# Kernel optimization log

Hardware: AMD Instinct MI355X
Metric: run time of the kernel (lower is better)

The kernel has to match this reference:

```python
import math
import jax, jax.numpy as jnp
from jax import lax
import numpy as np

LN_EPS = 1e-5
K = 3          # deform-conv kernel size
PAD = 1        # 'same' padding so offset map matches output resolution


def setup_inputs() -> dict:
    key = jax.random.key(0)
    ks = jax.random.split(key, 6)
    B, C, H, W, Co = 4, 256, 64, 64, 256
    x = jax.random.normal(ks[0], (B, C, H, W), jnp.float32)
    dwc_w = jax.random.normal(ks[1], (C, 1, K, K), jnp.float32) * 0.02
    ln_w = jnp.ones((C,), jnp.float32)
    ln_b = jnp.zeros((C,), jnp.float32)
    fcd_w = jax.random.normal(ks[2], (1, C, 1, 1), jnp.float32) * 0.02
    fca_w = jax.random.normal(ks[3], (1, C, 1, 1), jnp.float32) * 0.02
    fan_in = C * K * K
    dconv_w = jax.random.normal(ks[4], (Co, C, K, K), jnp.float32) / math.sqrt(fan_in)
    dconv_b = jnp.zeros((Co,), jnp.float32)
    return dict(x=x, dwc_w=dwc_w, ln_w=ln_w, ln_b=ln_b,
                fcd_w=fcd_w, fca_w=fca_w, dconv_w=dconv_w, dconv_b=dconv_b)


def _bilinear_sample(x, py, px):
    # x: [B,C,H,W]; py/px: [B,KK,H,W] float sample positions (zero-padded border)
    B, C, H, W = x.shape
    y0 = jnp.floor(py); x0 = jnp.floor(px)
    y1 = y0 + 1.0;      x1 = x0 + 1.0
    wy1 = py - y0; wy0 = 1.0 - wy1
    wx1 = px - x0; wx0 = 1.0 - wx1

    def gather(yy, xx):
        valid = ((yy >= 0) & (yy < H) & (xx >= 0) & (xx < W)).astype(x.dtype)
        iy = jnp.clip(yy, 0, H - 1).astype(jnp.int32)
        ix = jnp.clip(xx, 0, W - 1).astype(jnp.int32)
        # per-batch fancy gather -> [B,C,KK,H,W]
        v = jax.vmap(lambda img, a, b: img[:, a, b])(x, iy, ix)
        return v * valid[:, None]

    return (gather(y0, x0) * (wy0 * wx0)[:, None]
          + gather(y0, x1) * (wy0 * wx1)[:, None]
          + gather(y1, x0) * (wy1 * wx0)[:, None]
          + gather(y1, x1) * (wy1 * wx1)[:, None])


def reference(x, dwc_w, ln_w, ln_b, fcd_w, fca_w, dconv_w, dconv_b):
    B, C, H, W = x.shape
    KK = K * K
    # --- offset branch ---
    h = lax.conv_general_dilated(x, dwc_w, (1, 1), ((1, 1), (1, 1)),
                                 dimension_numbers=('NCHW', 'OIHW', 'NCHW'),
                                 feature_group_count=C)
    mu = h.mean(axis=1, keepdims=True)
    var = h.var(axis=1, keepdims=True)
    h = (h - mu) * lax.rsqrt(var + LN_EPS)
    h = h * ln_w[None, :, None, None] + ln_b[None, :, None, None]
    h = jax.nn.relu(h)
    r = jax.nn.relu(jnp.einsum('bchw,oc->bohw', h, fcd_w[:, :, 0, 0]))      # [B,1,H,W]
    t = jnp.einsum('bchw,oc->bohw', h, fca_w[:, :, 0, 0])
    theta = (t / (1.0 + jnp.abs(t))) * (math.pi / 180.0)                     # softsign * pi/180
    ox = r * jnp.cos(theta)
    oy = r * jnp.sin(theta)
    # torch code: offsets = cat([ox tiled KK, oy tiled KK], dim=1) -> [B,2KK,H,W]
    off = jnp.concatenate([jnp.tile(ox, (1, KK, 1, 1)), jnp.tile(oy, (1, KK, 1, 1))], axis=1)
    # torchvision DeformConv2d convention: channel 2k = dy, channel 2k+1 = dx
    dy = off[:, 0::2]   # [B,KK,H,W]
    dx = off[:, 1::2]
    # --- deformable sampling ---
    ky = jnp.repeat(jnp.arange(K), K).astype(x.dtype)   # kernel row per tap
    kx = jnp.tile(jnp.arange(K), K).astype(x.dtype)     # kernel col per tap
    py = (jnp.arange(H, dtype=x.dtype) - PAD)[None, None, :, None] + ky[None, :, None, None] + dy
    px = (jnp.arange(W, dtype=x.dtype) - PAD)[None, None, None, :] + kx[None, :, None, None] + dx
    sampled = _bilinear_sample(x, py, px)               # [B,C,KK,H,W]
    Co = dconv_w.shape[0]
    out = jnp.einsum('bckhw,ock->bohw', sampled, dconv_w.reshape(Co, C, KK))
    return out + dconv_b[None, :, None, None]
```

## Files before the change

kernel.cpp:

```cpp
#include <hip/hip_runtime.h>
#include <hip/hip_bf16.h>

#define B_   4
#define C_   256
#define CO_  256
#define H_   64
#define W_   64
#define HW_  4096

typedef __attribute__((ext_vector_type(8))) short short8;
typedef __attribute__((ext_vector_type(4))) float f32x4;
typedef __attribute__((ext_vector_type(2))) float f32x2;

static __device__ __forceinline__ unsigned short f2bf(float f) {
    unsigned u = __builtin_bit_cast(unsigned, f);
    unsigned r = (u + 0x7fffu + ((u >> 16) & 1u)) >> 16;
    return (unsigned short)r;
}
static __device__ __forceinline__ f32x2 pk_mul(f32x2 a, f32x2 b) {
    f32x2 d; asm("v_pk_mul_f32 %0, %1, %2" : "=v"(d) : "v"(a), "v"(b)); return d;
}
static __device__ __forceinline__ f32x2 pk_fma(f32x2 a, f32x2 b, f32x2 c) {
    f32x2 d; asm("v_pk_fma_f32 %0, %1, %2, %3" : "=v"(d) : "v"(a), "v"(b), "v"(c)); return d;
}
static __device__ __forceinline__ f32x2 pk_add(f32x2 a, f32x2 b) {
    f32x2 d; asm("v_pk_add_f32 %0, %1, %2" : "=v"(d) : "v"(a), "v"(b)); return d;
}
static __device__ __forceinline__ unsigned cvtpk(float a, float b) {
    unsigned r; asm("v_cvt_pk_bf16_f32 %0, %1, %2" : "=v"(r) : "v"(a), "v"(b)); return r;
}
static __device__ __forceinline__ f32x2 unpack_bf2(unsigned d) {
    f32x2 v;
    v.x = __builtin_bit_cast(float, d << 16);
    v.y = __builtin_bit_cast(float, d & 0xffff0000u);
    return v;
}

__global__ void k_pre(const float* __restrict__ x, unsigned short* __restrict__ xT,
                      const float* __restrict__ w, unsigned short* __restrict__ Bt,
                      const float* __restrict__ dwc_w, float* __restrict__ dwcT)
{
    int bid = blockIdx.x;
    int tid = threadIdx.x;
    if (bid < 1024) {
        __shared__ float t[32][132];
        int b   = bid >> 8;
        int rem = bid & 255;
        int hwT = rem >> 1, cT = rem & 1;
        int hw0 = hwT * 32, c0 = cT * 128;
        const float* src = x + (size_t)b * C_ * HW_;
        {
            int hw4 = (tid & 7) << 2;
            int cr  = tid >> 3;
#pragma unroll
            for (int it = 0; it < 4; ++it) {
                int c = cr + it * 32;
                f32x4 v = *(const f32x4*)(src + (size_t)(c0 + c) * HW_ + hw0 + hw4);
                t[hw4 + 0][c] = v.x;
                t[hw4 + 1][c] = v.y;
                t[hw4 + 2][c] = v.z;
                t[hw4 + 3][c] = v.w;
            }
        }
        __syncthreads();
        {
            int c8  = (tid & 15) << 3;
            int hwr = tid >> 4;
            unsigned short* dst = xT + (size_t)(((b << 12) + hw0) * 256) + c0 + c8;
#pragma unroll
            for (int it = 0; it < 2; ++it) {
                int hw = hwr + it * 16;
                f32x4 va = *(const f32x4*)&t[hw][c8];
                f32x4 vb = *(const f32x4*)&t[hw][c8 + 4];
                uint4 u;
                u.x = cvtpk(va.x, va.y);
                u.y = cvtpk(va.z, va.w);
                u.z = cvtpk(vb.x, vb.y);
                u.w = cvtpk(vb.z, vb.w);
                *(uint4*)(dst + (size_t)hw * 256) = u;
            }
        }
    } else {
        int pb = bid - 1024;
        if (pb < 9) dwcT[pb * 256 + tid] = dwc_w[tid * 9 + pb];
        int e = pb * 256 + tid;
        int j   = e & 7;
        int l4  = (e >> 3) & 3;
        int l15 = (e >> 5) & 15;
        int ks  = (e >> 9) & 7;
        int og  = (e >> 12) & 15;
        int k   = e >> 16;
        int o = og * 16 + l15;
        int c = ks * 32 + l4 * 8 + j;
        Bt[e] = f2bf(w[(o * C_ + c) * 9 + k]);
    }
}

__global__ void k_offsets(const unsigned short* __restrict__ xT,
                          const float* __restrict__ dwcT,
                          const float* __restrict__ ln_w,
                          const float* __restrict__ ln_b,
                          const float* __restrict__ fcd_w,
                          const float* __restrict__ fca_w,
                          float* __restrict__ OX, float* __restrict__ OY)
{
    int tid = threadIdx.x;
    int bi = blockIdx.x;
    int g = ((bi & 7) << 6) | (bi >> 3);
    int p0 = g << 5;
    int b = p0 >> 12;
    int y = (p0 >> 6) & 63;
    int xh = p0 & 63;
    int gpos = tid >> 4;
    int csub = tid & 15;
    int ch0 = csub << 4;
    const unsigned short* xb = xT + (size_t)b * HW_ * C_;

    f32x2 acc2[8];
#pragma unroll
    for (int i = 0; i < 8; ++i) { acc2[i].x = 0.f; acc2[i].y = 0.f; }
#pragma unroll
    for (int j = 0; j < 9; ++j) {
        int gy = y + j / 3 - 1, gx = xh + gpos + j % 3 - 1;
        if (gy >= 0 && gy < H_ && gx >= 0 && gx < W_) {
            const unsigned short* p = xb + (size_t)((gy << 6) + gx) * 256 + ch0;
            short8 rlo = *(const short8*)(p);
            short8 rhi = *(const short8*)(p + 8);
            const float* wrow = dwcT + j * 256 + ch0;
#pragma unroll
            for (int q = 0; q < 4; ++q) {
                f32x4 wv = *(const f32x4*)(wrow + q * 4);
                f32x2 w01v; w01v.x = wv.x; w01v.y = wv.y;
                f32x2 w23v; w23v.x = wv.z; w23v.y = wv.w;
                unsigned lo = (q < 2) ? ((unsigned*)&rlo)[q * 2] : ((unsigned*)&rhi)[(q - 2) * 2];
                unsigned hi = (q < 2) ? ((unsigned*)&rlo)[q * 2 + 1] : ((unsigned*)&rhi)[(q - 2) * 2 + 1];
                acc2[q * 2 + 0] = pk_fma(unpack_bf2(lo), w01v, acc2[q * 2 + 0]);
                acc2[q * 2 + 1] = pk_fma(unpack_bf2(hi), w23v, acc2[q * 2 + 1]);
            }
        }
    }
    f32x2 sum2, sq2;
    sum2.x = 0.f; sum2.y = 0.f; sq2.x = 0.f; sq2.y = 0.f;
#pragma unroll
    for (int i = 0; i < 8; ++i) {
        sum2 = pk_add(sum2, acc2[i]);
        sq2  = pk_fma(acc2[i], acc2[i], sq2);
    }
    float s1 = sum2.x + sum2.y, s2 = sq2.x + sq2.y;
#pragma unroll
    for (int m = 1; m <= 8; m <<= 1) {
        s1 += __shfl_xor(s1, m);
        s2 += __shfl_xor(s2, m);
    }
    float mu  = s1 * (1.f / 256.f);
    float var = s2 * (1.f / 256.f) - mu * mu;
    float rs  = rsqrtf(var + 1e-5f);
    float d1 = 0.f, d2 = 0.f;
#pragma unroll
    for (int q = 0; q < 4; ++q) {
        f32x4 lwv = *(const f32x4*)(ln_w  + ch0 + q * 4);
        f32x4 lbv = *(const f32x4*)(ln_b  + ch0 + q * 4);
        f32x4 fdv = *(const f32x4*)(fcd_w + ch0 + q * 4);
        f32x4 fav = *(const f32x4*)(fca_w + ch0 + q * 4);
#pragma unroll
        for (int i = 0; i < 4; ++i) {
            float av = (i & 1) ? acc2[q * 2 + (i >> 1)].y : acc2[q * 2 + (i >> 1)].x;
            float hn = (av - mu) * rs * lwv[i] + lbv[i];
            hn = fmaxf(hn, 0.f);
            d1 = fmaf(hn, fdv[i], d1);
            d2 = fmaf(hn, fav[i], d2);
        }
    }
#pragma unroll
    for (int m = 1; m <= 8; m <<= 1) {
        d1 += __shfl_xor(d1, m);
        d2 += __shfl_xor(d2, m);
    }
    if (csub == 0) {
        float r0 = fmaxf(d1, 0.f);
        float theta = d2 / (1.f + fabsf(d2)) * 0.017453292519943295f;
        int pos = p0 + gpos;
        OX[pos] = r0 * cosf(theta);
        OY[pos] = r0 * sinf(theta);
    }
}

__launch_bounds__(512, 4)
__global__ void k_main(const unsigned short* __restrict__ xT,
                       const float* __restrict__ OX, const float* __restrict__ OY,
                       const unsigned short* __restrict__ Bt,
                       const float* __restrict__ bias,
                       float* __restrict__ out)
{
    __shared__ __align__(16) unsigned char smem[32768];

    int tid = threadIdx.x;
    int bi = blockIdx.x;
    int g = ((bi & 7) << 6) | (bi >> 3);
    int tile = g >> 1;
    int n0g = g & 1;
    int b = tile >> 6;
    int y = tile & 63;

    int lane = tid & 63, wid = tid >> 6;
    int l15 = lane & 15, l4 = lane >> 4;

    f32x4 acc[4];
#pragma unroll
    for (int m = 0; m < 4; ++m) {
        acc[m].x = 0.f; acc[m].y = 0.f; acc[m].z = 0.f; acc[m].w = 0.f;
    }

    int gpos = tid >> 3;
    unsigned csub = (unsigned)tid & 7u;
    const char* xbB = (const char*)(xT + (size_t)b * HW_ * C_);
    const unsigned short* bwave = Bt + (unsigned)(n0g * 8 + wid) * 4096u
                                     + (unsigned)(l15 * 32 + l4 * 8);
    unsigned rowb = (unsigned)gpos * 256u;
    unsigned wsl0 = (csub ^ ((unsigned)gpos & 15u)) << 4;
    unsigned wsl1 = ((8u + csub) ^ ((unsigned)gpos & 15u)) << 4;
    float ox = OX[(tile << 6) + gpos], oy = OY[(tile << 6) + gpos];

    unsigned o00, o01, o10, o11;
    f32x2 W00, W01, W10, W11;

#define GADDR(k)                                                                  \
    {   int ky = (k) / 3, kx = (k) - ky * 3;                                      \
        float dyv = ((k) <= 4) ? ox : oy;                                         \
        float dxv = ((k) <= 3) ? ox : oy;                                         \
        float py = (float)(y - 1 + ky) + dyv;                                     \
        float px = (float)(gpos - 1 + kx) + dxv;                                  \
        float y0f = floorf(py), x0f = floorf(px);                                 \
        int y0 = (int)y0f, x0 = (int)x0f;                                         \
        int y1 = y0 + 1, x1 = x0 + 1;                                             \
        float wy1 = py - y0f, wy0 = 1.f - wy1;                                    \
        float wx1 = px - x0f, wx0 = 1.f - wx1;                                    \
        float vy0 = (y0 >= 0 && y0 < H_) ? 1.f : 0.f;                             \
        float vy1 = (y1 >= 0 && y1 < H_) ? 1.f : 0.f;                             \
        float vx0 = (x0 >= 0 && x0 < W_) ? 1.f : 0.f;                             \
        float vx1 = (x1 >= 0 && x1 < W_) ? 1.f : 0.f;                             \
        float w00 = wy0 * wx0 * vy0 * vx0, w01 = wy0 * wx1 * vy0 * vx1;           \
        float w10 = wy1 * wx0 * vy1 * vx0, w11 = wy1 * wx1 * vy1 * vx1;           \
        W00.x = w00; W00.y = w00; W01.x = w01; W01.y = w01;                       \
        W10.x = w10; W10.y = w10; W11.x = w11; W11.y = w11;                       \
        int y0c = min(max(y0, 0), H_ - 1), y1c = min(max(y1, 0), H_ - 1);         \
        int x0c = min(max(x0, 0), W_ - 1), x1c = min(max(x1, 0), W_ - 1);         \
        unsigned cb = csub << 4;                                                  \
        o00 = (unsigned)((y0c << 6) + x0c) * 512u + cb;                           \
        o01 = (unsigned)((y0c << 6) + x1c) * 512u + cb;                           \
        o10 = (unsigned)((y1c << 6) + x0c) * 512u + cb;                           \
        o11 = (unsigned)((y1c << 6) + x1c) * 512u + cb;                           \
    }

#define GATHER_HALF(h, hbase)                                                     \
    {   _Pragma("unroll")                                                         \
        for (int cq2 = 0; cq2 < 2; ++cq2) {                                       \
            unsigned gb = (unsigned)(h) * 256u + (unsigned)cq2 * 128u;            \
            short8 r00 = *(const short8*)(xbB + o00 + gb);                        \
            short8 r01 = *(const short8*)(xbB + o01 + gb);                        \
            short8 r10 = *(const short8*)(xbB + o10 + gb);                        \
            short8 r11 = *(const short8*)(xbB + o11 + gb);                        \
            uint4 pkv;                                                            \
            _Pragma("unroll")                                                     \
            for (int dw = 0; dw < 4; ++dw) {                                      \
                f32x2 a2 = pk_mul(unpack_bf2(((unsigned*)&r00)[dw]), W00);        \
                a2 = pk_fma(unpack_bf2(((unsigned*)&r01)[dw]), W01, a2);          \
                a2 = pk_fma(unpack_bf2(((unsigned*)&r10)[dw]), W10, a2);          \
                a2 = pk_fma(unpack_bf2(((unsigned*)&r11)[dw]), W11, a2);          \
                ((unsigned*)&pkv)[dw] = cvtpk(a2.x, a2.y);                        \
            }                                                                     \
            *(uint4*)(smem + (hbase) + rowb + (cq2 ? wsl1 : wsl0)) = pkv;         \
        }                                                                         \
    }

#define MFMA_HALF(k, h, hbase)                                                    \
    {   const unsigned short* bk = bwave + (unsigned)(k) * 65536u;                \
        _Pragma("unroll")                                                         \
        for (int ks2 = 0; ks2 < 4; ++ks2) {                                       \
            int ks = (h) * 4 + ks2;                                               \
            short8 bf = *(const short8*)(bk + ks * 512);                          \
            unsigned sl = ((unsigned)(ks2 * 4 + l4) ^ (unsigned)l15) << 4;        \
            _Pragma("unroll")                                                     \
            for (int mf = 0; mf < 4; ++mf) {                                      \
                unsigned row = (unsigned)(mf * 16 + l15);                         \
                short8 a = *(const short8*)(smem + (hbase) + row * 256u + sl);    \
                acc[mf] = __builtin_amdgcn_mfma_f32_16x16x32_bf16(a, bf, acc[mf], 0, 0, 0); \
            }                                                                     \
        }                                                                         \
    }

    GADDR(0);
    GATHER_HALF(0, 0u);
    __syncthreads();

#pragma unroll
    for (int k = 0; k < 9; ++k) {
        GATHER_HALF(1, 16384u);
        MFMA_HALF(k, 0, 0u);
        __syncthreads();
        if (k < 8) {
            GADDR(k + 1);
            GATHER_HALF(0, 0u);
        }
        MFMA_HALF(k, 1, 16384u);
        __syncthreads();
    }

    int col = n0g * 128 + wid * 16 + l15;
    float bv = bias[col];
    float* obase = out + ((size_t)(b * CO_ + col)) * HW_ + (y << 6);
#pragma unroll
    for (int mf = 0; mf < 4; ++mf) {
        f32x4 v;
        v.x = acc[mf].x + bv;
        v.y = acc[mf].y + bv;
        v.z = acc[mf].z + bv;
        v.w = acc[mf].w + bv;
        *(f32x4*)(obase + mf * 16 + l4 * 4) = v;
    }
}

extern "C" void kernel_launch(void* const* d_in, const int* in_sizes, int n_in,
                              void* d_out, int out_size, void* d_ws, size_t ws_size,
                              hipStream_t stream) {
    const float* x      = (const float*)d_in[0];
    const float* dwc_w  = (const float*)d_in[1];
    const float* ln_w   = (const float*)d_in[2];
    const float* ln_b   = (const float*)d_in[3];
    const float* fcd_w  = (const float*)d_in[4];
    const float* fca_w  = (const float*)d_in[5];
    const float* dconv_w= (const float*)d_in[6];
    const float* dconv_b= (const float*)d_in[7];
    float* out = (float*)d_out;

    unsigned char* ws = (unsigned char*)d_ws;
    unsigned short* xT = (unsigned short*)(ws);
    unsigned short* Bt = (unsigned short*)(ws + 8388608);
    float* dwcT        = (float*)(ws + 9568256);
    float* OX          = (float*)(ws + 9577472);
    float* OY          = (float*)(ws + 9643008);

    k_pre<<<3328, 256, 0, stream>>>(x, xT, dconv_w, Bt, dwc_w, dwcT);
    k_offsets<<<512, 512, 0, stream>>>(xT, dwcT, ln_w, ln_b, fcd_w, fca_w, OX, OY);
    k_main<<<512, 512, 0, stream>>>(xT, OX, OY, Bt, dconv_b, out);
}
```

Baseline: 73.49 us.

## Retile deform-conv main kernel to 32-pixel by 256-channel tiles with 1024 threads

```diff
diff --git a/kernel.cpp b/kernel.cpp
--- a/kernel.cpp
+++ b/kernel.cpp
@@ -185,7 +185,7 @@
     }
 }
 
-__launch_bounds__(512, 4)
+__launch_bounds__(1024, 8)
 __global__ void k_main(const unsigned short* __restrict__ xT,
                        const float* __restrict__ OX, const float* __restrict__ OY,
                        const unsigned short* __restrict__ Bt,
@@ -197,29 +197,28 @@
     int tid = threadIdx.x;
     int bi = blockIdx.x;
     int g = ((bi & 7) << 6) | (bi >> 3);
-    int tile = g >> 1;
-    int n0g = g & 1;
-    int b = tile >> 6;
-    int y = tile & 63;
+    int p0 = g << 5;
+    int b = p0 >> 12;
+    int y = (p0 >> 6) & 63;
+    int xh = p0 & 63;
 
     int lane = tid & 63, wid = tid >> 6;
     int l15 = lane & 15, l4 = lane >> 4;
 
-    f32x4 acc[4];
-#pragma unroll
-    for (int m = 0; m < 4; ++m) {
+    f32x4 acc[2];
+#pragma unroll
+    for (int m = 0; m < 2; ++m) {
         acc[m].x = 0.f; acc[m].y = 0.f; acc[m].z = 0.f; acc[m].w = 0.f;
     }
 
-    int gpos = tid >> 3;
-    unsigned csub = (unsigned)tid & 7u;
+    int gpos = tid >> 5;
+    unsigned csub = (unsigned)tid & 31u;
     const char* xbB = (const char*)(xT + (size_t)b * HW_ * C_);
-    const unsigned short* bwave = Bt + (unsigned)(n0g * 8 + wid) * 4096u
+    const unsigned short* bwave = Bt + (unsigned)wid * 4096u
                                      + (unsigned)(l15 * 32 + l4 * 8);
-    unsigned rowb = (unsigned)gpos * 256u;
-    unsigned wsl0 = (csub ^ ((unsigned)gpos & 15u)) << 4;
-    unsigned wsl1 = ((8u + csub) ^ ((unsigned)gpos & 15u)) << 4;
-    float ox = OX[(tile << 6) + gpos], oy = OY[(tile << 6) + gpos];
+    unsigned rowb = (unsigned)gpos * 512u;
+    unsigned wsl  = (csub ^ ((unsigned)gpos & 15u)) << 4;
+    float ox = OX[p0 + gpos], oy = OY[p0 + gpos];
 
     unsigned o00, o01, o10, o11;
     f32x2 W00, W01, W10, W11;
@@ -229,7 +228,7 @@
         float dyv = ((k) <= 4) ? ox : oy;                                         \
         float dxv = ((k) <= 3) ? ox : oy;                                         \
         float py = (float)(y - 1 + ky) + dyv;                                     \
-        float px = (float)(gpos - 1 + kx) + dxv;                                  \
+        float px = (float)(xh + gpos - 1 + kx) + dxv;                             \
         float y0f = floorf(py), x0f = floorf(px);                                 \
         int y0 = (int)y0f, x0 = (int)x0f;                                         \
         int y1 = y0 + 1, x1 = x0 + 1;                                             \
@@ -252,65 +251,59 @@
         o11 = (unsigned)((y1c << 6) + x1c) * 512u + cb;                           \
     }
 
-#define GATHER_HALF(h, hbase)                                                     \
-    {   _Pragma("unroll")                                                         \
-        for (int cq2 = 0; cq2 < 2; ++cq2) {                                       \
-            unsigned gb = (unsigned)(h) * 256u + (unsigned)cq2 * 128u;            \
-            short8 r00 = *(const short8*)(xbB + o00 + gb);                        \
-            short8 r01 = *(const short8*)(xbB + o01 + gb);                        \
-            short8 r10 = *(const short8*)(xbB + o10 + gb);                        \
-            short8 r11 = *(const short8*)(xbB + o11 + gb);                        \
-            uint4 pkv;                                                            \
-            _Pragma("unroll")                                                     \
-            for (int dw = 0; dw < 4; ++dw) {                                      \
-                f32x2 a2 = pk_mul(unpack_bf2(((unsigned*)&r00)[dw]), W00);        \
-                a2 = pk_fma(unpack_bf2(((unsigned*)&r01)[dw]), W01, a2);          \
-                a2 = pk_fma(unpack_bf2(((unsigned*)&r10)[dw]), W10, a2);          \
-                a2 = pk_fma(unpack_bf2(((unsigned*)&r11)[dw]), W11, a2);          \
-                ((unsigned*)&pkv)[dw] = cvtpk(a2.x, a2.y);                        \
-            }                                                                     \
-            *(uint4*)(smem + (hbase) + rowb + (cq2 ? wsl1 : wsl0)) = pkv;         \
+#define GATHER_TAP(hbase)                                                         \
+    {   short8 r00 = *(const short8*)(xbB + o00);                                 \
+        short8 r01 = *(const short8*)(xbB + o01);                                 \
+        short8 r10 = *(const short8*)(xbB + o10);                                 \
+        short8 r11 = *(const short8*)(xbB + o11);                                 \
+        uint4 pkv;                                                                \
+        _Pragma("unroll")                                                         \
+        for (int dw = 0; dw < 4; ++dw) {                                          \
+            f32x2 a2 = pk_mul(unpack_bf2(((unsigned*)&r00)[dw]), W00);            \
+            a2 = pk_fma(unpack_bf2(((unsigned*)&r01)[dw]), W01, a2);              \
+            a2 = pk_fma(unpack_bf2(((unsigned*)&r10)[dw]), W10, a2);              \
+            a2 = pk_fma(unpack_bf2(((unsigned*)&r11)[dw]), W11, a2);              \
+            ((unsigned*)&pkv)[dw] = cvtpk(a2.x, a2.y);                            \
         }                                                                         \
-    }
-
-#define MFMA_HALF(k, h, hbase)                                                    \
+        *(uint4*)(smem + (hbase) + rowb + wsl) = pkv;                             \
+    }
+
+#define MFMA_TAP(k, hbase)                                                        \
     {   const unsigned short* bk = bwave + (unsigned)(k) * 65536u;                \
         _Pragma("unroll")                                                         \
-        for (int ks2 = 0; ks2 < 4; ++ks2) {                                       \
-            int ks = (h) * 4 + ks2;                                               \
+        for (int ks = 0; ks < 8; ++ks) {                                          \
             short8 bf = *(const short8*)(bk + ks * 512);                          \
-            unsigned sl = ((unsigned)(ks2 * 4 + l4) ^ (unsigned)l15) << 4;        \
+            unsigned sl = ((unsigned)(ks * 4 + l4) ^ (unsigned)l15) << 4;         \
             _Pragma("unroll")                                                     \
-            for (int mf = 0; mf < 4; ++mf) {                                      \
+            for (int mf = 0; mf < 2; ++mf) {                                      \
                 unsigned row = (unsigned)(mf * 16 + l15);                         \
-                short8 a = *(const short8*)(smem + (hbase) + row * 256u + sl);    \
+                short8 a = *(const short8*)(smem + (hbase) + row * 512u + sl);    \
                 acc[mf] = __builtin_amdgcn_mfma_f32_16x16x32_bf16(a, bf, acc[mf], 0, 0, 0); \
             }                                                                     \
         }                                                                         \
     }
 
     GADDR(0);
-    GATHER_HALF(0, 0u);
+    GATHER_TAP(0u);
     __syncthreads();
 
 #pragma unroll
     for (int k = 0; k < 9; ++k) {
-        GATHER_HALF(1, 16384u);
-        MFMA_HALF(k, 0, 0u);
-        __syncthreads();
+        unsigned cur = (k & 1) ? 16384u : 0u;
+        unsigned nxt = (k & 1) ? 0u : 16384u;
         if (k < 8) {
             GADDR(k + 1);
-            GATHER_HALF(0, 0u);
-        }
-        MFMA_HALF(k, 1, 16384u);
+            GATHER_TAP(nxt);
+        }
+        MFMA_TAP(k, cur);
         __syncthreads();
     }
 
-    int col = n0g * 128 + wid * 16 + l15;
+    int col = wid * 16 + l15;
     float bv = bias[col];
-    float* obase = out + ((size_t)(b * CO_ + col)) * HW_ + (y << 6);
-#pragma unroll
-    for (int mf = 0; mf < 4; ++mf) {
+    float* obase = out + ((size_t)(b * CO_ + col)) * HW_ + (y << 6) + xh;
+#pragma unroll
+    for (int mf = 0; mf < 2; ++mf) {
         f32x4 v;
         v.x = acc[mf].x + bv;
         v.y = acc[mf].y + bv;
@@ -342,5 +335,5 @@
 
     k_pre<<<3328, 256, 0, stream>>>(x, xT, dconv_w, Bt, dwc_w, dwcT);
     k_offsets<<<512, 512, 0, stream>>>(xT, dwcT, ln_w, ln_b, fcd_w, fca_w, OX, OY);
-    k_main<<<512, 512, 0, stream>>>(xT, OX, OY, Bt, dconv_b, out);
-}
+    k_main<<<512, 1024, 0, stream>>>(xT, OX, OY, Bt, dconv_b, out);
+}
```

After: 80.25 us. +9.2%, slower.

## Compute all output channels per block and double-buffer full-tap gathers

Applied to the files above, without the earlier changes.

```diff
diff --git a/kernel.cpp b/kernel.cpp
--- a/kernel.cpp
+++ b/kernel.cpp
@@ -185,36 +185,36 @@
     }
 }
 
-__launch_bounds__(512, 4)
+__launch_bounds__(512, 2)
 __global__ void k_main(const unsigned short* __restrict__ xT,
                        const float* __restrict__ OX, const float* __restrict__ OY,
                        const unsigned short* __restrict__ Bt,
                        const float* __restrict__ bias,
                        float* __restrict__ out)
 {
-    __shared__ __align__(16) unsigned char smem[32768];
+    __shared__ __align__(16) unsigned char smem[65536];
 
     int tid = threadIdx.x;
     int bi = blockIdx.x;
-    int g = ((bi & 7) << 6) | (bi >> 3);
-    int tile = g >> 1;
-    int n0g = g & 1;
+    int tile = ((bi & 7) << 5) | (bi >> 3);
     int b = tile >> 6;
     int y = tile & 63;
 
     int lane = tid & 63, wid = tid >> 6;
     int l15 = lane & 15, l4 = lane >> 4;
 
-    f32x4 acc[4];
-#pragma unroll
-    for (int m = 0; m < 4; ++m) {
-        acc[m].x = 0.f; acc[m].y = 0.f; acc[m].z = 0.f; acc[m].w = 0.f;
-    }
+    f32x4 acc[4][2];
+#pragma unroll
+    for (int m = 0; m < 4; ++m)
+#pragma unroll
+        for (int n = 0; n < 2; ++n) {
+            acc[m][n].x = 0.f; acc[m][n].y = 0.f; acc[m][n].z = 0.f; acc[m][n].w = 0.f;
+        }
 
     int gpos = tid >> 3;
     unsigned csub = (unsigned)tid & 7u;
     const char* xbB = (const char*)(xT + (size_t)b * HW_ * C_);
-    const unsigned short* bwave = Bt + (unsigned)(n0g * 8 + wid) * 4096u
+    const unsigned short* bwave = Bt + (unsigned)(wid * 2) * 4096u
                                      + (unsigned)(l15 * 32 + l4 * 8);
     unsigned rowb = (unsigned)gpos * 256u;
     unsigned wsl0 = (csub ^ ((unsigned)gpos & 15u)) << 4;
@@ -278,45 +278,52 @@
         _Pragma("unroll")                                                         \
         for (int ks2 = 0; ks2 < 4; ++ks2) {                                       \
             int ks = (h) * 4 + ks2;                                               \
-            short8 bf = *(const short8*)(bk + ks * 512);                          \
+            short8 bf0 = *(const short8*)(bk + ks * 512);                         \
+            short8 bf1 = *(const short8*)(bk + 4096 + ks * 512);                  \
             unsigned sl = ((unsigned)(ks2 * 4 + l4) ^ (unsigned)l15) << 4;        \
             _Pragma("unroll")                                                     \
             for (int mf = 0; mf < 4; ++mf) {                                      \
                 unsigned row = (unsigned)(mf * 16 + l15);                         \
                 short8 a = *(const short8*)(smem + (hbase) + row * 256u + sl);    \
-                acc[mf] = __builtin_amdgcn_mfma_f32_16x16x32_bf16(a, bf, acc[mf], 0, 0, 0); \
+                acc[mf][0] = __builtin_amdgcn_mfma_f32_16x16x32_bf16(a, bf0, acc[mf][0], 0, 0, 0); \
+                acc[mf][1] = __builtin_amdgcn_mfma_f32_16x16x32_bf16(a, bf1, acc[mf][1], 0, 0, 0); \
             }                                                                     \
         }                                                                         \
     }
 
     GADDR(0);
     GATHER_HALF(0, 0u);
+    GATHER_HALF(1, 16384u);
     __syncthreads();
 
 #pragma unroll
     for (int k = 0; k < 9; ++k) {
-        GATHER_HALF(1, 16384u);
-        MFMA_HALF(k, 0, 0u);
-        __syncthreads();
+        unsigned cur = (k & 1) ? 32768u : 0u;
+        unsigned nxt = (k & 1) ? 0u : 32768u;
         if (k < 8) {
             GADDR(k + 1);
-            GATHER_HALF(0, 0u);
-        }
-        MFMA_HALF(k, 1, 16384u);
+            GATHER_HALF(0, nxt);
+            GATHER_HALF(1, nxt + 16384u);
+        }
+        MFMA_HALF(k, 0, cur);
+        MFMA_HALF(k, 1, cur + 16384u);
         __syncthreads();
     }
 
-    int col = n0g * 128 + wid * 16 + l15;
-    float bv = bias[col];
-    float* obase = out + ((size_t)(b * CO_ + col)) * HW_ + (y << 6);
-#pragma unroll
-    for (int mf = 0; mf < 4; ++mf) {
-        f32x4 v;
-        v.x = acc[mf].x + bv;
-        v.y = acc[mf].y + bv;
-        v.z = acc[mf].z + bv;
-        v.w = acc[mf].w + bv;
-        *(f32x4*)(obase + mf * 16 + l4 * 4) = v;
+#pragma unroll
+    for (int nf = 0; nf < 2; ++nf) {
+        int col = wid * 32 + nf * 16 + l15;
+        float bv = bias[col];
+        float* obase = out + ((size_t)(b * CO_ + col)) * HW_ + (y << 6);
+#pragma unroll
+        for (int mf = 0; mf < 4; ++mf) {
+            f32x4 v;
+            v.x = acc[mf][nf].x + bv;
+            v.y = acc[mf][nf].y + bv;
+            v.z = acc[mf][nf].z + bv;
+            v.w = acc[mf][nf].w + bv;
+            *(f32x4*)(obase + mf * 16 + l4 * 4) = v;
+        }
     }
 }
 
@@ -342,5 +349,5 @@
 
     k_pre<<<3328, 256, 0, stream>>>(x, xT, dconv_w, Bt, dwc_w, dwcT);
     k_offsets<<<512, 512, 0, stream>>>(xT, dwcT, ln_w, ln_b, fcd_w, fca_w, OX, OY);
-    k_main<<<512, 512, 0, stream>>>(xT, OX, OY, Bt, dconv_b, out);
-}
+    k_main<<<256, 512, 0, stream>>>(xT, OX, OY, Bt, dconv_b, out);
+}
```

Result: faster. 69.19 us, median of 2 (-5.8%).
